# Performance work log

Hardware: AMD Instinct MI355X
Metric: run time of the kernel (lower is better)

The kernel has to match this reference:

```python
import jax, jax.numpy as jnp
import numpy as np

B, N, CPTS = 16, 4096, 64
M, K, RADIUS = 1024, 32, 0.2
MLP = [64, 64, 128]
EPS = 1e-5  # torch BatchNorm2d default


def setup_inputs() -> dict:
    key = jax.random.key(0)
    ks = jax.random.split(key, 2 + len(MLP))
    inp = {
        "xyz": jax.random.uniform(ks[0], (B, N, 3), dtype=jnp.float32),
        "points": jax.random.normal(ks[1], (B, N, CPTS), dtype=jnp.float32),
    }
    cin = 3 + CPTS
    for i, cout in enumerate(MLP):
        inp[f"W{i}"] = jax.random.normal(ks[2 + i], (cout, cin), dtype=jnp.float32) / np.sqrt(cin)
        inp[f"g{i}"] = jnp.ones((cout,), jnp.float32)
        inp[f"b{i}"] = jnp.zeros((cout,), jnp.float32)
        cin = cout
    return inp


def fps(xyz, m):
    # Farthest point sampling, deterministic start at index 0. Returns (B, m) int32.
    b, n, _ = xyz.shape

    def step(carry, _):
        min_d, far = carry
        cent = jnp.take_along_axis(xyz, far[:, None, None], axis=1)  # (B,1,3)
        d = jnp.sum((xyz - cent) ** 2, axis=-1)                      # (B,N)
        min_d = jnp.minimum(min_d, d)
        return (min_d, jnp.argmax(min_d, axis=-1).astype(jnp.int32)), far

    init = (jnp.full((b, n), 1e10, xyz.dtype), jnp.zeros((b,), jnp.int32))
    _, inds = jax.lax.scan(step, init, None, length=m)
    return inds.T  # (B, m)


def ball_query(xyz, new_xyz, radius, k):
    # Euclidean distances (B,M,N); indices within radius, first-k, pad with first valid.
    d2 = (jnp.sum(new_xyz ** 2, -1)[:, :, None] + jnp.sum(xyz ** 2, -1)[:, None, :]
          - 2.0 * jnp.einsum('bmc,bnc->bmn', new_xyz, xyz))
    dists = jnp.sqrt(jnp.maximum(d2, 0.0))
    n = xyz.shape[1]
    idx = jnp.where(dists > radius, n, jnp.arange(n, dtype=jnp.int32)[None, None, :])
    idx = jnp.sort(idx, axis=-1)[:, :, :k]          # first k in-radius indices (N-padded)
    first = idx[:, :, :1]                           # centroid itself (dist 0) always valid
    return jnp.where(idx == n, first, idx)          # (B, M, k)


def reference(xyz, points, W0, g0, b0, W1, g1, b1, W2, g2, b2):
    bidx = jnp.arange(B)[:, None]
    fps_inds = fps(xyz, M)                          # (B, M)
    new_xyz = xyz[bidx, fps_inds]                   # (B, M, 3)
    g_inds = ball_query(xyz, new_xyz, RADIUS, K)    # (B, M, K)
    bidx2 = jnp.arange(B)[:, None, None]
    grouped_xyz = xyz[bidx2, g_inds] - new_xyz[:, :, None, :]   # (B,M,K,3) local coords
    grouped_pts = points[bidx2, g_inds]                          # (B,M,K,C)
    feats = jnp.concatenate([grouped_xyz, grouped_pts], axis=-1)  # (B,M,K,3+C)

    # 1x1 Conv2d (no bias) + BatchNorm2d (training-mode batch stats) + ReLU
    for Wi, gi, bi in ((W0, g0, b0), (W1, g1, b1), (W2, g2, b2)):
        h = jnp.einsum('bmkc,oc->bmko', feats, Wi)
        mean = h.mean(axis=(0, 1, 2))
        var = h.var(axis=(0, 1, 2))
        feats = jax.nn.relu(gi * (h - mean) * jax.lax.rsqrt(var + EPS) + bi)

    new_points = feats.max(axis=2)                  # max-pool over K -> (B, M, 128)
    return new_xyz, new_points, g_inds
```

## Files before the change

kernel.cpp:

```cpp
#include <hip/hip_runtime.h>
#include <hip/hip_bf16.h>
#include <cstdint>

#define B_ 16
#define N_ 4096
#define CPTS_ 64
#define M_ 1024
#define K_ 32
#define MF_TOT 2097152

using ushort8 = __attribute__((ext_vector_type(8))) unsigned short;
using bf16x8  = __attribute__((ext_vector_type(8))) short;
using f32x4v  = __attribute__((ext_vector_type(4))) float;

static __device__ __forceinline__ unsigned f2bf(float x){
  unsigned u = __float_as_uint(x);
  return (u + 0x7fffu + ((u >> 16) & 1u)) >> 16;
}
static __device__ __forceinline__ float bf2f(unsigned short u){
  return __uint_as_float(((unsigned)u) << 16);
}

#define DPPMAX(v, ctrl)                                                        \
  do {                                                                         \
    int _t = __builtin_amdgcn_update_dpp(0, __float_as_int(v), (ctrl), 0xf,    \
                                         0xf, true);                           \
    (v) = fmaxf((v), __int_as_float(_t));                                      \
  } while (0)

#define STEP(MD, PX, PY, PZ, C, J)                                             \
  { float dx = PX.C - cx, dy = PY.C - cy, dz = PZ.C - cz;                      \
    float d = dx * dx; d = d + dy * dy; d = d + dz * dz;                       \
    float nm = fminf(MD.C, d); MD.C = nm;                                      \
    if (nm > bv){ bv = nm; bj = (J); } }
#define STEP4(MD, PX, PY, PZ, J0)                                              \
  STEP(MD, PX, PY, PZ, x, J0)                                                  \
  STEP(MD, PX, PY, PZ, y, (J0) + 1)                                            \
  STEP(MD, PX, PY, PZ, z, (J0) + 2)                                            \
  STEP(MD, PX, PY, PZ, w, (J0) + 3)

__global__ __launch_bounds__(256, 1) void fps_kernel(const float* __restrict__ xyz,
                                                     float* __restrict__ newxyz){
#pragma clang fp contract(off)
  __shared__ float xs[N_], ys[N_], zs[N_];
  __shared__ int inds_s[M_];
  __shared__ unsigned long long sv_[2][4];
  const int b = blockIdx.x, tid = threadIdx.x;
  const int lane = tid & 63, wv = tid >> 6;
  const float* xb = xyz + (size_t)b * N_ * 3;
  for (int i = tid; i < N_ * 3; i += 256){
    float v = xb[i];
    int n = i / 3, c = i - n * 3;
    if (c == 0) xs[n] = v; else if (c == 1) ys[n] = v; else zs[n] = v;
  }
  __syncthreads();
  const float4 px0 = *reinterpret_cast<const float4*>(&xs[tid * 16 + 0]);
  const float4 px1 = *reinterpret_cast<const float4*>(&xs[tid * 16 + 4]);
  const float4 px2 = *reinterpret_cast<const float4*>(&xs[tid * 16 + 8]);
  const float4 px3 = *reinterpret_cast<const float4*>(&xs[tid * 16 + 12]);
  const float4 py0 = *reinterpret_cast<const float4*>(&ys[tid * 16 + 0]);
  const float4 py1 = *reinterpret_cast<const float4*>(&ys[tid * 16 + 4]);
  const float4 py2 = *reinterpret_cast<const float4*>(&ys[tid * 16 + 8]);
  const float4 py3 = *reinterpret_cast<const float4*>(&ys[tid * 16 + 12]);
  const float4 pz0 = *reinterpret_cast<const float4*>(&zs[tid * 16 + 0]);
  const float4 pz1 = *reinterpret_cast<const float4*>(&zs[tid * 16 + 4]);
  const float4 pz2 = *reinterpret_cast<const float4*>(&zs[tid * 16 + 8]);
  const float4 pz3 = *reinterpret_cast<const float4*>(&zs[tid * 16 + 12]);
  float4 md0 = make_float4(1e10f, 1e10f, 1e10f, 1e10f);
  float4 md1 = md0, md2 = md0, md3 = md0;
  int far = 0;
  float cx = xs[0], cy = ys[0], cz = zs[0];
  for (int m = 0; m < M_; ++m){
    if (tid == 0) inds_s[m] = far;
    float bv = -1.0f; int bj = 0;
    STEP4(md0, px0, py0, pz0, 0)
    STEP4(md1, px1, py1, pz1, 4)
    STEP4(md2, px2, py2, pz2, 8)
    STEP4(md3, px3, py3, pz3, 12)
    float wm = bv;
    DPPMAX(wm, 0x111);
    DPPMAX(wm, 0x112);
    DPPMAX(wm, 0x114);
    DPPMAX(wm, 0x118);
    DPPMAX(wm, 0x142);
    DPPMAX(wm, 0x143);
    const float wmax = __int_as_float(
        __builtin_amdgcn_readlane(__float_as_int(wm), 63));
    unsigned long long tied = __ballot(bv == wmax);
    const int winlane = (int)__builtin_ctzll(tied);
    const int sl = m & 1;
    if (lane == winlane){
      int wn = tid * 16 + bj;
      sv_[sl][wv] = ((unsigned long long)__float_as_uint(wmax) << 32)
                  | (unsigned)(4095 - wn);
    }
    __syncthreads();
    unsigned long long p0 = sv_[sl][0], p1 = sv_[sl][1], p2 = sv_[sl][2], p3 = sv_[sl][3];
    if (p1 > p0) p0 = p1;
    if (p3 > p2) p2 = p3;
    if (p2 > p0) p0 = p2;
    far = 4095 - (int)(p0 & 0xffffffffu);
    cx = xs[far]; cy = ys[far]; cz = zs[far];
  }
  __syncthreads();
  for (int t = tid; t < M_; t += 256){
    int id = inds_s[t];
    size_t o = ((size_t)b * M_ + t) * 3;
    newxyz[o] = xs[id]; newxyz[o + 1] = ys[id]; newxyz[o + 2] = zs[id];
  }
}

__global__ __launch_bounds__(256) void phi_kernel(const float* __restrict__ xyz,
                                                  const float* __restrict__ points,
                                                  const float* __restrict__ W,
                                                  float* __restrict__ phi){
  __shared__ __align__(16) float Wt[67][64];
  __shared__ __align__(16) float ft[67][128];
  const int tid = threadIdx.x, blk = blockIdx.x;
  const int p0 = blk * 128;
  for (int i = tid; i < 67 * 64; i += 256){
    int o = i / 67, c = i - o * 67;
    Wt[c][o] = W[i];
  }
  const int sl = tid >> 1, half = tid & 1;
  const int p = p0 + sl;
  const float* ps = points + (size_t)p * CPTS_ + half * 32;
  #pragma unroll
  for (int j = 0; j < 8; ++j){
    float4 v = *reinterpret_cast<const float4*>(ps + j * 4);
    int c = 3 + half * 32 + j * 4;
    ft[c][sl] = v.x; ft[c + 1][sl] = v.y; ft[c + 2][sl] = v.z; ft[c + 3][sl] = v.w;
  }
  if (half == 0){
    const float* xp = xyz + (size_t)p * 3;
    ft[0][sl] = xp[0]; ft[1][sl] = xp[1]; ft[2][sl] = xp[2];
  }
  __syncthreads();
  const int sg = tid & 31, og = tid >> 5;
  float acc[4][8];
  #pragma unroll
  for (int i = 0; i < 4; ++i)
    #pragma unroll
    for (int o = 0; o < 8; ++o) acc[i][o] = 0.0f;
  #pragma unroll 2
  for (int c = 0; c < 67; ++c){
    float4 f = *reinterpret_cast<const float4*>(&ft[c][sg * 4]);
    float4 w0 = *reinterpret_cast<const float4*>(&Wt[c][og * 8]);
    float4 w1 = *reinterpret_cast<const float4*>(&Wt[c][og * 8 + 4]);
    const float fv[4] = {f.x, f.y, f.z, f.w};
    #pragma unroll
    for (int i = 0; i < 4; ++i){
      acc[i][0] += fv[i] * w0.x; acc[i][1] += fv[i] * w0.y;
      acc[i][2] += fv[i] * w0.z; acc[i][3] += fv[i] * w0.w;
      acc[i][4] += fv[i] * w1.x; acc[i][5] += fv[i] * w1.y;
      acc[i][6] += fv[i] * w1.z; acc[i][7] += fv[i] * w1.w;
    }
  }
  #pragma unroll
  for (int i = 0; i < 4; ++i){
    float* dst = phi + (size_t)(p0 + sg * 4 + i) * 64 + og * 8;
    *reinterpret_cast<float4*>(dst)     = make_float4(acc[i][0], acc[i][1], acc[i][2], acc[i][3]);
    *reinterpret_cast<float4*>(dst + 4) = make_float4(acc[i][4], acc[i][5], acc[i][6], acc[i][7]);
  }
}

__global__ __launch_bounds__(256) void ballq_psi_kernel(const float* __restrict__ xyz,
                                                        const float* __restrict__ newxyz,
                                                        int* __restrict__ gi,
                                                        float* __restrict__ gif,
                                                        const float* __restrict__ W0,
                                                        float* __restrict__ psi){
  if (blockIdx.x >= 4096){
    const int mi = (blockIdx.x - 4096) * 256 + threadIdx.x;
    const float x = newxyz[(size_t)mi * 3];
    const float y = newxyz[(size_t)mi * 3 + 1];
    const float z = newxyz[(size_t)mi * 3 + 2];
    float* dst = psi + (size_t)mi * 64;
    #pragma unroll
    for (int o4 = 0; o4 < 16; ++o4){
      float v[4];
      #pragma unroll
      for (int e = 0; e < 4; ++e){
        int o = o4 * 4 + e;
        v[e] = fmaf(z, W0[o * 67 + 2], fmaf(y, W0[o * 67 + 1], x * W0[o * 67]));
      }
      *reinterpret_cast<float4*>(dst + o4 * 4) = make_float4(v[0], v[1], v[2], v[3]);
    }
    return;
  }
  const int gw = (blockIdx.x * 256 + threadIdx.x) >> 6;
  const int lane = threadIdx.x & 63;
  const int b = gw >> 10, m = gw & 1023;
  const float* xb = xyz + (size_t)b * N_ * 3;
  const size_t no = (size_t)b * M_ + m;
  const float cx = newxyz[no * 3], cy = newxyz[no * 3 + 1], cz = newxyz[no * 3 + 2];
  const float sm = fmaf(cz, cz, fmaf(cy, cy, cx * cx));
  int total = 0, first_idx = 0; bool havef = false;
  int*   gd = gi  + no * K_;
  float* fd = gif + no * K_;
  for (int ch = 0; ch < 64 && total < K_; ++ch){
    const int n = ch * 64 + lane;
    const float x = xb[n * 3], y = xb[n * 3 + 1], z = xb[n * 3 + 2];
    const float sn = fmaf(z, z, fmaf(y, y, x * x));
    const float dt = fmaf(z, cz, fmaf(y, cy, x * cx));
    float d2 = (sm + sn) - 2.0f * dt;
    float dist = sqrtf(fmaxf(d2, 0.0f));
    bool pred = !(dist > 0.2f);
    unsigned long long mask = __ballot(pred);
    if (!havef && mask){ havef = true; first_idx = ch * 64 + (int)__builtin_ctzll(mask); }
    if (pred){
      int rank = total + (int)__popcll(mask & ((1ull << lane) - 1ull));
      if (rank < K_){ gd[rank] = n; fd[rank] = (float)n; }
    }
    total += (int)__popcll(mask);
  }
  if (total < K_ && lane >= total && lane < K_){ gd[lane] = first_idx; fd[lane] = (float)first_idx; }
}

__global__ __launch_bounds__(256) void stats0_kernel(const float* __restrict__ phi,
                                                     const float* __restrict__ psi,
                                                     const int* __restrict__ gi,
                                                     float* __restrict__ part){
  __shared__ int gidx[128];
  __shared__ float psm[4][64];
  const int tid = threadIdx.x, blk = blockIdx.x;
  const size_t s0 = (size_t)blk * 128;
  const int b  = (int)(s0 >> 15);
  const int m0 = ((int)(s0 & 32767)) >> 5;
  if (tid < 128) gidx[tid] = gi[(size_t)b * 32768 + (size_t)m0 * K_ + tid];
  psm[tid >> 6][tid & 63] =
      psi[((size_t)b * M_ + m0 + (tid >> 6)) * 64 + (tid & 63)];
  __syncthreads();
  const int sg = tid & 31, og = tid >> 5;
  const int mi = sg >> 3;
  float sv[8], sq[8];
  #pragma unroll
  for (int o = 0; o < 8; ++o){ sv[o] = 0.f; sq[o] = 0.f; }
  #pragma unroll
  for (int i = 0; i < 4; ++i){
    const int g = gidx[sg * 4 + i];
    const float* gp = phi + ((size_t)b * N_ + g) * 64 + og * 8;
    float4 a0 = *reinterpret_cast<const float4*>(gp);
    float4 a1 = *reinterpret_cast<const float4*>(gp + 4);
    const float pv[8] = {a0.x, a0.y, a0.z, a0.w, a1.x, a1.y, a1.z, a1.w};
    #pragma unroll
    for (int o = 0; o < 8; ++o){
      float v = pv[o] - psm[mi][og * 8 + o];
      sv[o] += v; sq[o] += v * v;
    }
  }
  #pragma unroll
  for (int off = 1; off < 32; off <<= 1){
    #pragma unroll
    for (int o = 0; o < 8; ++o){
      sv[o] += __shfl_xor(sv[o], off);
      sq[o] += __shfl_xor(sq[o], off);
    }
  }
  if (sg == 0){
    #pragma unroll
    for (int o = 0; o < 8; ++o){
      int ch = og * 8 + o;
      part[(size_t)(ch * 2) * 4096 + blk]     = sv[o];
      part[(size_t)(ch * 2 + 1) * 4096 + blk] = sq[o];
    }
  }
}

__global__ __launch_bounds__(256) void mlp1_mfma(
    const float* __restrict__ phi, const float* __restrict__ psi,
    const int* __restrict__ gi, const float* __restrict__ bn0,
    const float* __restrict__ W1,
    unsigned short* __restrict__ h1, float* __restrict__ part)
{
  __shared__ unsigned short wsh[64 * 72], wsl[64 * 72];
  __shared__ unsigned short fsh[128 * 72], fsl[128 * 72];
  __shared__ int gidx[128];
  __shared__ float psm[4][64];
  const int tid = threadIdx.x, blk = blockIdx.x;
  const size_t s0 = (size_t)blk * 128;
  const int b  = (int)(s0 >> 15);
  const int m0 = ((int)(s0 & 32767)) >> 5;

  for (int i = tid; i < 64 * 64; i += 256){
    int o = i >> 6, c = i & 63;
    float f = W1[i];
    unsigned hb = f2bf(f);
    float res = f - bf2f((unsigned short)hb);
    wsh[o * 72 + c] = (unsigned short)hb;
    wsl[o * 72 + c] = (unsigned short)f2bf(res);
  }
  if (tid < 128) gidx[tid] = gi[(size_t)b * 32768 + (size_t)m0 * K_ + tid];
  psm[tid >> 6][tid & 63] =
      psi[((size_t)b * M_ + m0 + (tid >> 6)) * 64 + (tid & 63)];
  __syncthreads();
  {
    const int sl = tid >> 1, half = tid & 1;
    const int g = gidx[sl];
    const int mi = sl >> 5;
    const float* gp = phi + ((size_t)b * N_ + g) * 64 + half * 32;
    #pragma unroll
    for (int jj = 0; jj < 4; ++jj){
      float4 v0 = *reinterpret_cast<const float4*>(gp + jj * 8);
      float4 v1 = *reinterpret_cast<const float4*>(gp + jj * 8 + 4);
      const float vv[8] = {v0.x, v0.y, v0.z, v0.w, v1.x, v1.y, v1.z, v1.w};
      ushort8 ph, pl;
      #pragma unroll
      for (int e = 0; e < 8; ++e){
        int c = half * 32 + jj * 8 + e;
        float f = fmaxf((vv[e] - psm[mi][c]) * bn0[c] + bn0[64 + c], 0.0f);
        unsigned hb = f2bf(f);
        float res = f - bf2f((unsigned short)hb);
        ph[e] = (unsigned short)hb;
        pl[e] = (unsigned short)f2bf(res);
      }
      *reinterpret_cast<ushort8*>(&fsh[sl * 72 + half * 32 + jj * 8]) = ph;
      *reinterpret_cast<ushort8*>(&fsl[sl * 72 + half * 32 + jj * 8]) = pl;
    }
  }
  __syncthreads();

  const int l = tid & 63, w = tid >> 6;
  const int col = l & 15, g4 = l >> 4;
  const int ch = w * 16 + col;

  bf16x8 bh[2], bl[2];
  #pragma unroll
  for (int ks = 0; ks < 2; ++ks){
    int a = ch * 72 + ks * 32 + g4 * 8;
    bh[ks] = *reinterpret_cast<const bf16x8*>(&wsh[a]);
    bl[ks] = *reinterpret_cast<const bf16x8*>(&wsl[a]);
  }

  f32x4v acc[8];
  #pragma unroll
  for (int st = 0; st < 8; ++st) acc[st] = (f32x4v){0.f, 0.f, 0.f, 0.f};

  #pragma unroll
  for (int st = 0; st < 8; ++st){
    #pragma unroll
    for (int ks = 0; ks < 2; ++ks){
      int a = (st * 16 + col) * 72 + ks * 32 + g4 * 8;
      bf16x8 ah = *reinterpret_cast<const bf16x8*>(&fsh[a]);
      bf16x8 al = *reinterpret_cast<const bf16x8*>(&fsl[a]);
      acc[st] = __builtin_amdgcn_mfma_f32_16x16x32_bf16(ah, bh[ks], acc[st], 0, 0, 0);
      acc[st] = __builtin_amdgcn_mfma_f32_16x16x32_bf16(ah, bl[ks], acc[st], 0, 0, 0);
      acc[st] = __builtin_amdgcn_mfma_f32_16x16x32_bf16(al, bh[ks], acc[st], 0, 0, 0);
    }
  }

  #pragma unroll
  for (int st = 0; st < 8; ++st){
    size_t sbase = s0 + st * 16 + g4 * 4;
    #pragma unroll
    for (int r = 0; r < 4; ++r)
      h1[(sbase + r) * 64 + ch] = (unsigned short)f2bf(acc[st][r]);
  }

  float sv = 0.f, sq = 0.f;
  #pragma unroll
  for (int st = 0; st < 8; ++st){
    f32x4v a = acc[st];
    float t0 = a[0], t1 = a[1], t2 = a[2], t3 = a[3];
    sv += ((t0 + t1) + t2) + t3;
    sq += ((t0 * t0 + t1 * t1) + t2 * t2) + t3 * t3;
  }
  sv += __shfl_xor(sv, 16); sv += __shfl_xor(sv, 32);
  sq += __shfl_xor(sq, 16); sq += __shfl_xor(sq, 32);
  if (g4 == 0){
    part[(size_t)(ch * 2) * 4096 + blk]     = sv;
    part[(size_t)(ch * 2 + 1) * 4096 + blk] = sq;
  }
}

__global__ __launch_bounds__(256) void mlp2_mfma(
    const unsigned short* __restrict__ h1, const float* __restrict__ bn1,
    const float* __restrict__ W2, float* __restrict__ part,
    float* __restrict__ mxmn)
{
  __shared__ unsigned short wsh[128 * 72], wsl[128 * 72];
  __shared__ unsigned short fsh[128 * 72], fsl[128 * 72];
  const int tid = threadIdx.x, blk = blockIdx.x;
  const size_t s0 = (size_t)blk * 128;

  for (int i = tid; i < 128 * 64; i += 256){
    int o = i >> 6, c = i & 63;
    float f = W2[i];
    unsigned hb = f2bf(f);
    float res = f - bf2f((unsigned short)hb);
    wsh[o * 72 + c] = (unsigned short)hb;
    wsl[o * 72 + c] = (unsigned short)f2bf(res);
  }
  {
    const int sl = tid >> 1, c0 = (tid & 1) * 32;
    const unsigned short* hp = h1 + (s0 + sl) * 64 + c0;
    #pragma unroll
    for (int j = 0; j < 4; ++j){
      ushort8 raw = *reinterpret_cast<const ushort8*>(hp + j * 8);
      ushort8 ph, pl;
      #pragma unroll
      for (int e = 0; e < 8; ++e){
        int c = c0 + j * 8 + e;
        float f = fmaxf(bf2f(raw[e]) * bn1[c] + bn1[64 + c], 0.0f);
        unsigned hb = f2bf(f);
        float res = f - bf2f((unsigned short)hb);
        ph[e] = (unsigned short)hb;
        pl[e] = (unsigned short)f2bf(res);
      }
      *reinterpret_cast<ushort8*>(&fsh[sl * 72 + c0 + j * 8]) = ph;
      *reinterpret_cast<ushort8*>(&fsl[sl * 72 + c0 + j * 8]) = pl;
    }
  }
  __syncthreads();

  const int l = tid & 63, w = tid >> 6;
  const int col = l & 15, g = l >> 4;

  bf16x8 bh[2][2], bl[2][2];
  #pragma unroll
  for (int ot = 0; ot < 2; ++ot)
    #pragma unroll
    for (int ks = 0; ks < 2; ++ks){
      int a = (w * 32 + ot * 16 + col) * 72 + ks * 32 + g * 8;
      bh[ot][ks] = *reinterpret_cast<const bf16x8*>(&wsh[a]);
      bl[ot][ks] = *reinterpret_cast<const bf16x8*>(&wsl[a]);
    }

  f32x4v acc[8][2];
  #pragma unroll
  for (int st = 0; st < 8; ++st)
    #pragma unroll
    for (int ot = 0; ot < 2; ++ot)
      acc[st][ot] = (f32x4v){0.f, 0.f, 0.f, 0.f};

  #pragma unroll
  for (int st = 0; st < 8; ++st){
    bf16x8 ah[2], al[2];
    #pragma unroll
    for (int ks = 0; ks < 2; ++ks){
      int a = (st * 16 + col) * 72 + ks * 32 + g * 8;
      ah[ks] = *reinterpret_cast<const bf16x8*>(&fsh[a]);
      al[ks] = *reinterpret_cast<const bf16x8*>(&fsl[a]);
    }
    #pragma unroll
    for (int ot = 0; ot < 2; ++ot){
      #pragma unroll
      for (int ks = 0; ks < 2; ++ks){
        acc[st][ot] = __builtin_amdgcn_mfma_f32_16x16x32_bf16(ah[ks], bh[ot][ks], acc[st][ot], 0, 0, 0);
        acc[st][ot] = __builtin_amdgcn_mfma_f32_16x16x32_bf16(ah[ks], bl[ot][ks], acc[st][ot], 0, 0, 0);
        acc[st][ot] = __builtin_amdgcn_mfma_f32_16x16x32_bf16(al[ks], bh[ot][ks], acc[st][ot], 0, 0, 0);
      }
    }
  }

  #pragma unroll
  for (int ot = 0; ot < 2; ++ot){
    const int ch = w * 32 + ot * 16 + col;
    float sv = 0.f, sq = 0.f;
    float mxm[4], mnm[4];
    #pragma unroll
    for (int j = 0; j < 4; ++j){ mxm[j] = -1e30f; mnm[j] = 1e30f; }
    #pragma unroll
    for (int st = 0; st < 8; ++st){
      f32x4v a = acc[st][ot];
      float t0 = a[0], t1 = a[1], t2 = a[2], t3 = a[3];
      sv += ((t0 + t1) + t2) + t3;
      sq += ((t0 * t0 + t1 * t1) + t2 * t2) + t3 * t3;
      float tmx = fmaxf(fmaxf(t0, t1), fmaxf(t2, t3));
      float tmn = fminf(fminf(t0, t1), fminf(t2, t3));
      mxm[st >> 1] = fmaxf(mxm[st >> 1], tmx);
      mnm[st >> 1] = fminf(mnm[st >> 1], tmn);
    }
    sv += __shfl_xor(sv, 16); sv += __shfl_xor(sv, 32);
    sq += __shfl_xor(sq, 16); sq += __shfl_xor(sq, 32);
    #pragma unroll
    for (int j = 0; j < 4; ++j){
      mxm[j] = fmaxf(mxm[j], __shfl_xor(mxm[j], 16));
      mxm[j] = fmaxf(mxm[j], __shfl_xor(mxm[j], 32));
      mnm[j] = fminf(mnm[j], __shfl_xor(mnm[j], 16));
      mnm[j] = fminf(mnm[j], __shfl_xor(mnm[j], 32));
    }
    if (g == 0){
      part[(size_t)(ch * 2) * 4096 + blk]     = sv;
      part[(size_t)(ch * 2 + 1) * 4096 + blk] = sq;
      #pragma unroll
      for (int j = 0; j < 4; ++j){
        size_t mf = (s0 >> 5) + j;
        mxmn[mf * 128 + ch]          = mxm[j];
        mxmn[MF_TOT + mf * 128 + ch] = mnm[j];
      }
    }
  }
}

__global__ __launch_bounds__(256) void reduce_stats(const float* __restrict__ part,
                                                    const float* __restrict__ g,
                                                    const float* __restrict__ bb,
                                                    float* __restrict__ bn, int cout){
  const int ch = blockIdx.x, tid = threadIdx.x;
  float s = 0.f, q = 0.f;
  const float* ps = part + (size_t)(ch * 2) * 4096;
  const float* pq = part + (size_t)(ch * 2 + 1) * 4096;
  for (int i = tid; i < 4096; i += 256){ s += ps[i]; q += pq[i]; }
  #pragma unroll
  for (int off = 1; off < 64; off <<= 1){ s += __shfl_xor(s, off); q += __shfl_xor(q, off); }
  __shared__ float as_[4], aq_[4];
  if ((tid & 63) == 0){ as_[tid >> 6] = s; aq_[tid >> 6] = q; }
  __syncthreads();
  if (tid == 0){
    float S = as_[0] + as_[1] + as_[2] + as_[3];
    float Q = aq_[0] + aq_[1] + aq_[2] + aq_[3];
    const float cnt = 524288.0f;
    float mean = S / cnt;
    float var  = Q / cnt - mean * mean;
    float sc = g[ch] / sqrtf(var + 1e-5f);
    bn[ch] = sc;
    bn[cout + ch] = bb[ch] - mean * sc;
  }
}

__global__ __launch_bounds__(256) void bn_minmax_finish(const float* __restrict__ mxmn,
                                                        const float* __restrict__ bn2,
                                                        float* __restrict__ out){
  const int i = blockIdx.x * 256 + threadIdx.x;
  const int ch = i & 127;
  const float a = bn2[ch], sh = bn2[128 + ch];
  const float mx = mxmn[i], mn = mxmn[MF_TOT + i];
  out[i] = fmaxf(fmaxf(mx * a + sh, mn * a + sh), 0.0f);
}

extern "C" void kernel_launch(void* const* d_in, const int* in_sizes, int n_in,
                              void* d_out, int out_size, void* d_ws, size_t ws_size,
                              hipStream_t stream){
  (void)in_sizes; (void)n_in; (void)out_size; (void)ws_size;
  const float* xyz    = (const float*)d_in[0];
  const float* points = (const float*)d_in[1];
  const float* W0 = (const float*)d_in[2];
  const float* g0 = (const float*)d_in[3];
  const float* b0 = (const float*)d_in[4];
  const float* W1 = (const float*)d_in[5];
  const float* g1 = (const float*)d_in[6];
  const float* b1 = (const float*)d_in[7];
  const float* W2 = (const float*)d_in[8];
  const float* g2 = (const float*)d_in[9];
  const float* b2 = (const float*)d_in[10];

  float* out = (float*)d_out;
  float* o_newxyz = out;
  float* o_newpts = out + (size_t)B_ * M_ * 3;
  float* o_gind   = out + (size_t)B_ * M_ * 3 + (size_t)B_ * M_ * 128;

  char* ws = (char*)d_ws;
  int*   gi   = (int*)(ws + 0);
  float* part = (float*)(ws + (2ull << 20));
  float* bn0  = (float*)(ws + (6ull << 20));
  float* bn1  = (float*)(ws + (6ull << 20) + 1024);
  float* bn2  = (float*)(ws + (6ull << 20) + 2048);
  float* phi  = (float*)(ws + (8ull << 20));
  float* psi  = (float*)(ws + (24ull << 20));
  unsigned short* h1 = (unsigned short*)(ws + (28ull << 20));
  float* mxmn = (float*)(ws + (92ull << 20));

  phi_kernel<<<512, 256, 0, stream>>>(xyz, points, W0, phi);
  fps_kernel<<<16, 256, 0, stream>>>(xyz, o_newxyz);
  ballq_psi_kernel<<<4160, 256, 0, stream>>>(xyz, o_newxyz, gi, o_gind, W0, psi);

  stats0_kernel<<<4096, 256, 0, stream>>>(phi, psi, gi, part);
  reduce_stats<<<64, 256, 0, stream>>>(part, g0, b0, bn0, 64);

  mlp1_mfma<<<4096, 256, 0, stream>>>(phi, psi, gi, bn0, W1, h1, part);
  reduce_stats<<<64, 256, 0, stream>>>(part, g1, b1, bn1, 64);

  mlp2_mfma<<<4096, 256, 0, stream>>>(h1, bn1, W2, part, mxmn);
  reduce_stats<<<128, 256, 0, stream>>>(part, g2, b2, bn2, 128);
  bn_minmax_finish<<<MF_TOT / 256, 256, 0, stream>>>(mxmn, bn2, o_newpts);
}
```

Baseline: 876.2 us.

## Fuse phi into FPS launch and fold layer-0 stats into ball query

The phi projection blocks now run in the same launch as the 16 FPS blocks, so phi can fill the idle CUs while the long serial FPS loop runs instead of executing as a separate kernel. The ball query kernel keeps each wave's neighbour indices in shared memory and computes the per-centroid layer-0 sum and sum-of-squares right away, which removes the separate stats0 kernel and its reread of gi. A new row-major reduce kernel reduces these per-wave partials. The cost is a larger partial buffer (16384x64 values each for sum and sum-of-squares) and a gathered phi read per wave inside the ball query kernel.

```diff
diff --git a/kernel.cpp b/kernel.cpp
--- a/kernel.cpp
+++ b/kernel.cpp
@@ -8,6 +8,7 @@
 #define M_ 1024
 #define K_ 32
 #define MF_TOT 2097152
+#define NW_ 16384
 
 using ushort8 = __attribute__((ext_vector_type(8))) unsigned short;
 using bf16x8  = __attribute__((ext_vector_type(8))) short;
@@ -39,137 +40,142 @@
   STEP(MD, PX, PY, PZ, z, (J0) + 2)                                            \
   STEP(MD, PX, PY, PZ, w, (J0) + 3)
 
-__global__ __launch_bounds__(256, 1) void fps_kernel(const float* __restrict__ xyz,
-                                                     float* __restrict__ newxyz){
+__global__ __launch_bounds__(256, 1) void fps_phi_kernel(
+    const float* __restrict__ xyz, float* __restrict__ newxyz,
+    const float* __restrict__ points, const float* __restrict__ W,
+    float* __restrict__ phi){
+  __shared__ __align__(16) char smem[53760];
+  if (blockIdx.x >= 16){
+    float* Wt = (float*)smem;
+    float* ft = (float*)(smem + 17152);
+    const int tid = threadIdx.x, blk = blockIdx.x - 16;
+    const int p0 = blk * 128;
+    for (int i = tid; i < 67 * 64; i += 256){
+      int o = i / 67, c = i - o * 67;
+      Wt[c * 64 + o] = W[i];
+    }
+    const int sl = tid >> 1, half = tid & 1;
+    const int p = p0 + sl;
+    const float* ps = points + (size_t)p * CPTS_ + half * 32;
+    #pragma unroll
+    for (int j = 0; j < 8; ++j){
+      float4 v = *reinterpret_cast<const float4*>(ps + j * 4);
+      int c = 3 + half * 32 + j * 4;
+      ft[c * 128 + sl] = v.x; ft[(c + 1) * 128 + sl] = v.y;
+      ft[(c + 2) * 128 + sl] = v.z; ft[(c + 3) * 128 + sl] = v.w;
+    }
+    if (half == 0){
+      const float* xp = xyz + (size_t)p * 3;
+      ft[0 * 128 + sl] = xp[0]; ft[1 * 128 + sl] = xp[1]; ft[2 * 128 + sl] = xp[2];
+    }
+    __syncthreads();
+    const int sg = tid & 31, og = tid >> 5;
+    float acc[4][8];
+    #pragma unroll
+    for (int i = 0; i < 4; ++i)
+      #pragma unroll
+      for (int o = 0; o < 8; ++o) acc[i][o] = 0.0f;
+    #pragma unroll 2
+    for (int c = 0; c < 67; ++c){
+      float4 f = *reinterpret_cast<const float4*>(&ft[c * 128 + sg * 4]);
+      float4 w0 = *reinterpret_cast<const float4*>(&Wt[c * 64 + og * 8]);
+      float4 w1 = *reinterpret_cast<const float4*>(&Wt[c * 64 + og * 8 + 4]);
+      const float fv[4] = {f.x, f.y, f.z, f.w};
+      #pragma unroll
+      for (int i = 0; i < 4; ++i){
+        acc[i][0] += fv[i] * w0.x; acc[i][1] += fv[i] * w0.y;
+        acc[i][2] += fv[i] * w0.z; acc[i][3] += fv[i] * w0.w;
+        acc[i][4] += fv[i] * w1.x; acc[i][5] += fv[i] * w1.y;
+        acc[i][6] += fv[i] * w1.z; acc[i][7] += fv[i] * w1.w;
+      }
+    }
+    #pragma unroll
+    for (int i = 0; i < 4; ++i){
+      float* dst = phi + (size_t)(p0 + sg * 4 + i) * 64 + og * 8;
+      *reinterpret_cast<float4*>(dst)     = make_float4(acc[i][0], acc[i][1], acc[i][2], acc[i][3]);
+      *reinterpret_cast<float4*>(dst + 4) = make_float4(acc[i][4], acc[i][5], acc[i][6], acc[i][7]);
+    }
+    return;
+  }
+  {
 #pragma clang fp contract(off)
-  __shared__ float xs[N_], ys[N_], zs[N_];
-  __shared__ int inds_s[M_];
-  __shared__ unsigned long long sv_[2][4];
-  const int b = blockIdx.x, tid = threadIdx.x;
-  const int lane = tid & 63, wv = tid >> 6;
-  const float* xb = xyz + (size_t)b * N_ * 3;
-  for (int i = tid; i < N_ * 3; i += 256){
-    float v = xb[i];
-    int n = i / 3, c = i - n * 3;
-    if (c == 0) xs[n] = v; else if (c == 1) ys[n] = v; else zs[n] = v;
-  }
-  __syncthreads();
-  const float4 px0 = *reinterpret_cast<const float4*>(&xs[tid * 16 + 0]);
-  const float4 px1 = *reinterpret_cast<const float4*>(&xs[tid * 16 + 4]);
-  const float4 px2 = *reinterpret_cast<const float4*>(&xs[tid * 16 + 8]);
-  const float4 px3 = *reinterpret_cast<const float4*>(&xs[tid * 16 + 12]);
-  const float4 py0 = *reinterpret_cast<const float4*>(&ys[tid * 16 + 0]);
-  const float4 py1 = *reinterpret_cast<const float4*>(&ys[tid * 16 + 4]);
-  const float4 py2 = *reinterpret_cast<const float4*>(&ys[tid * 16 + 8]);
-  const float4 py3 = *reinterpret_cast<const float4*>(&ys[tid * 16 + 12]);
-  const float4 pz0 = *reinterpret_cast<const float4*>(&zs[tid * 16 + 0]);
-  const float4 pz1 = *reinterpret_cast<const float4*>(&zs[tid * 16 + 4]);
-  const float4 pz2 = *reinterpret_cast<const float4*>(&zs[tid * 16 + 8]);
-  const float4 pz3 = *reinterpret_cast<const float4*>(&zs[tid * 16 + 12]);
-  float4 md0 = make_float4(1e10f, 1e10f, 1e10f, 1e10f);
-  float4 md1 = md0, md2 = md0, md3 = md0;
-  int far = 0;
-  float cx = xs[0], cy = ys[0], cz = zs[0];
-  for (int m = 0; m < M_; ++m){
-    if (tid == 0) inds_s[m] = far;
-    float bv = -1.0f; int bj = 0;
-    STEP4(md0, px0, py0, pz0, 0)
-    STEP4(md1, px1, py1, pz1, 4)
-    STEP4(md2, px2, py2, pz2, 8)
-    STEP4(md3, px3, py3, pz3, 12)
-    float wm = bv;
-    DPPMAX(wm, 0x111);
-    DPPMAX(wm, 0x112);
-    DPPMAX(wm, 0x114);
-    DPPMAX(wm, 0x118);
-    DPPMAX(wm, 0x142);
-    DPPMAX(wm, 0x143);
-    const float wmax = __int_as_float(
-        __builtin_amdgcn_readlane(__float_as_int(wm), 63));
-    unsigned long long tied = __ballot(bv == wmax);
-    const int winlane = (int)__builtin_ctzll(tied);
-    const int sl = m & 1;
-    if (lane == winlane){
-      int wn = tid * 16 + bj;
-      sv_[sl][wv] = ((unsigned long long)__float_as_uint(wmax) << 32)
-                  | (unsigned)(4095 - wn);
+    float* xs = (float*)smem;
+    float* ys = (float*)(smem + 16384);
+    float* zs = (float*)(smem + 32768);
+    int* inds_s = (int*)(smem + 49152);
+    unsigned long long* sv_ = (unsigned long long*)(smem + 53248);
+    const int b = blockIdx.x, tid = threadIdx.x;
+    const int lane = tid & 63, wv = tid >> 6;
+    const float* xb = xyz + (size_t)b * N_ * 3;
+    for (int i = tid; i < N_ * 3; i += 256){
+      float v = xb[i];
+      int n = i / 3, c = i - n * 3;
+      if (c == 0) xs[n] = v; else if (c == 1) ys[n] = v; else zs[n] = v;
     }
     __syncthreads();
-    unsigned long long p0 = sv_[sl][0], p1 = sv_[sl][1], p2 = sv_[sl][2], p3 = sv_[sl][3];
-    if (p1 > p0) p0 = p1;
-    if (p3 > p2) p2 = p3;
-    if (p2 > p0) p0 = p2;
-    far = 4095 - (int)(p0 & 0xffffffffu);
-    cx = xs[far]; cy = ys[far]; cz = zs[far];
-  }
-  __syncthreads();
-  for (int t = tid; t < M_; t += 256){
-    int id = inds_s[t];
-    size_t o = ((size_t)b * M_ + t) * 3;
-    newxyz[o] = xs[id]; newxyz[o + 1] = ys[id]; newxyz[o + 2] = zs[id];
-  }
-}
-
-__global__ __launch_bounds__(256) void phi_kernel(const float* __restrict__ xyz,
-                                                  const float* __restrict__ points,
-                                                  const float* __restrict__ W,
-                                                  float* __restrict__ phi){
-  __shared__ __align__(16) float Wt[67][64];
-  __shared__ __align__(16) float ft[67][128];
-  const int tid = threadIdx.x, blk = blockIdx.x;
-  const int p0 = blk * 128;
-  for (int i = tid; i < 67 * 64; i += 256){
-    int o = i / 67, c = i - o * 67;
-    Wt[c][o] = W[i];
-  }
-  const int sl = tid >> 1, half = tid & 1;
-  const int p = p0 + sl;
-  const float* ps = points + (size_t)p * CPTS_ + half * 32;
-  #pragma unroll
-  for (int j = 0; j < 8; ++j){
-    float4 v = *reinterpret_cast<const float4*>(ps + j * 4);
-    int c = 3 + half * 32 + j * 4;
-    ft[c][sl] = v.x; ft[c + 1][sl] = v.y; ft[c + 2][sl] = v.z; ft[c + 3][sl] = v.w;
-  }
-  if (half == 0){
-    const float* xp = xyz + (size_t)p * 3;
-    ft[0][sl] = xp[0]; ft[1][sl] = xp[1]; ft[2][sl] = xp[2];
-  }
-  __syncthreads();
-  const int sg = tid & 31, og = tid >> 5;
-  float acc[4][8];
-  #pragma unroll
-  for (int i = 0; i < 4; ++i)
-    #pragma unroll
-    for (int o = 0; o < 8; ++o) acc[i][o] = 0.0f;
-  #pragma unroll 2
-  for (int c = 0; c < 67; ++c){
-    float4 f = *reinterpret_cast<const float4*>(&ft[c][sg * 4]);
-    float4 w0 = *reinterpret_cast<const float4*>(&Wt[c][og * 8]);
-    float4 w1 = *reinterpret_cast<const float4*>(&Wt[c][og * 8 + 4]);
-    const float fv[4] = {f.x, f.y, f.z, f.w};
-    #pragma unroll
-    for (int i = 0; i < 4; ++i){
-      acc[i][0] += fv[i] * w0.x; acc[i][1] += fv[i] * w0.y;
-      acc[i][2] += fv[i] * w0.z; acc[i][3] += fv[i] * w0.w;
-      acc[i][4] += fv[i] * w1.x; acc[i][5] += fv[i] * w1.y;
-      acc[i][6] += fv[i] * w1.z; acc[i][7] += fv[i] * w1.w;
-    }
-  }
-  #pragma unroll
-  for (int i = 0; i < 4; ++i){
-    float* dst = phi + (size_t)(p0 + sg * 4 + i) * 64 + og * 8;
-    *reinterpret_cast<float4*>(dst)     = make_float4(acc[i][0], acc[i][1], acc[i][2], acc[i][3]);
-    *reinterpret_cast<float4*>(dst + 4) = make_float4(acc[i][4], acc[i][5], acc[i][6], acc[i][7]);
-  }
-}
-
-__global__ __launch_bounds__(256) void ballq_psi_kernel(const float* __restrict__ xyz,
-                                                        const float* __restrict__ newxyz,
-                                                        int* __restrict__ gi,
-                                                        float* __restrict__ gif,
-                                                        const float* __restrict__ W0,
-                                                        float* __restrict__ psi){
+    const float4 px0 = *reinterpret_cast<const float4*>(&xs[tid * 16 + 0]);
+    const float4 px1 = *reinterpret_cast<const float4*>(&xs[tid * 16 + 4]);
+    const float4 px2 = *reinterpret_cast<const float4*>(&xs[tid * 16 + 8]);
+    const float4 px3 = *reinterpret_cast<const float4*>(&xs[tid * 16 + 12]);
+    const float4 py0 = *reinterpret_cast<const float4*>(&ys[tid * 16 + 0]);
+    const float4 py1 = *reinterpret_cast<const float4*>(&ys[tid * 16 + 4]);
+    const float4 py2 = *reinterpret_cast<const float4*>(&ys[tid * 16 + 8]);
+    const float4 py3 = *reinterpret_cast<const float4*>(&ys[tid * 16 + 12]);
+    const float4 pz0 = *reinterpret_cast<const float4*>(&zs[tid * 16 + 0]);
+    const float4 pz1 = *reinterpret_cast<const float4*>(&zs[tid * 16 + 4]);
+    const float4 pz2 = *reinterpret_cast<const float4*>(&zs[tid * 16 + 8]);
+    const float4 pz3 = *reinterpret_cast<const float4*>(&zs[tid * 16 + 12]);
+    float4 md0 = make_float4(1e10f, 1e10f, 1e10f, 1e10f);
+    float4 md1 = md0, md2 = md0, md3 = md0;
+    int far = 0;
+    float cx = xs[0], cy = ys[0], cz = zs[0];
+    for (int m = 0; m < M_; ++m){
+      if (tid == 0) inds_s[m] = far;
+      float bv = -1.0f; int bj = 0;
+      STEP4(md0, px0, py0, pz0, 0)
+      STEP4(md1, px1, py1, pz1, 4)
+      STEP4(md2, px2, py2, pz2, 8)
+      STEP4(md3, px3, py3, pz3, 12)
+      float wm = bv;
+      DPPMAX(wm, 0x111);
+      DPPMAX(wm, 0x112);
+      DPPMAX(wm, 0x114);
+      DPPMAX(wm, 0x118);
+      DPPMAX(wm, 0x142);
+      DPPMAX(wm, 0x143);
+      const float wmax = __int_as_float(
+          __builtin_amdgcn_readlane(__float_as_int(wm), 63));
+      unsigned long long tied = __ballot(bv == wmax);
+      const int winlane = (int)__builtin_ctzll(tied);
+      const int sl = m & 1;
+      if (lane == winlane){
+        int wn = tid * 16 + bj;
+        sv_[sl * 4 + wv] = ((unsigned long long)__float_as_uint(wmax) << 32)
+                         | (unsigned)(4095 - wn);
+      }
+      __syncthreads();
+      unsigned long long p0 = sv_[sl * 4 + 0], p1 = sv_[sl * 4 + 1];
+      unsigned long long p2 = sv_[sl * 4 + 2], p3 = sv_[sl * 4 + 3];
+      if (p1 > p0) p0 = p1;
+      if (p3 > p2) p2 = p3;
+      if (p2 > p0) p0 = p2;
+      far = 4095 - (int)(p0 & 0xffffffffu);
+      cx = xs[far]; cy = ys[far]; cz = zs[far];
+    }
+    __syncthreads();
+    for (int t = tid; t < M_; t += 256){
+      int id = inds_s[t];
+      size_t o = ((size_t)b * M_ + t) * 3;
+      newxyz[o] = xs[id]; newxyz[o + 1] = ys[id]; newxyz[o + 2] = zs[id];
+    }
+  }
+}
+
+__global__ __launch_bounds__(256) void ballq_stats_kernel(
+    const float* __restrict__ xyz, const float* __restrict__ newxyz,
+    int* __restrict__ gi, float* __restrict__ gif,
+    const float* __restrict__ W0, float* __restrict__ psi,
+    const float* __restrict__ phi, float* __restrict__ part0){
   if (blockIdx.x >= 4096){
     const int mi = (blockIdx.x - 4096) * 256 + threadIdx.x;
     const float x = newxyz[(size_t)mi * 3];
@@ -188,6 +194,8 @@
     }
     return;
   }
+  __shared__ int sidx[4][K_];
+  const int wvb = threadIdx.x >> 6;
   const int gw = (blockIdx.x * 256 + threadIdx.x) >> 6;
   const int lane = threadIdx.x & 63;
   const int b = gw >> 10, m = gw & 1023;
@@ -210,60 +218,51 @@
     if (!havef && mask){ havef = true; first_idx = ch * 64 + (int)__builtin_ctzll(mask); }
     if (pred){
       int rank = total + (int)__popcll(mask & ((1ull << lane) - 1ull));
-      if (rank < K_){ gd[rank] = n; fd[rank] = (float)n; }
+      if (rank < K_){ gd[rank] = n; fd[rank] = (float)n; sidx[wvb][rank] = n; }
     }
     total += (int)__popcll(mask);
   }
-  if (total < K_ && lane >= total && lane < K_){ gd[lane] = first_idx; fd[lane] = (float)first_idx; }
-}
-
-__global__ __launch_bounds__(256) void stats0_kernel(const float* __restrict__ phi,
-                                                     const float* __restrict__ psi,
-                                                     const int* __restrict__ gi,
-                                                     float* __restrict__ part){
-  __shared__ int gidx[128];
-  __shared__ float psm[4][64];
-  const int tid = threadIdx.x, blk = blockIdx.x;
-  const size_t s0 = (size_t)blk * 128;
-  const int b  = (int)(s0 >> 15);
-  const int m0 = ((int)(s0 & 32767)) >> 5;
-  if (tid < 128) gidx[tid] = gi[(size_t)b * 32768 + (size_t)m0 * K_ + tid];
-  psm[tid >> 6][tid & 63] =
-      psi[((size_t)b * M_ + m0 + (tid >> 6)) * 64 + (tid & 63)];
+  if (total < K_ && lane >= total && lane < K_){
+    gd[lane] = first_idx; fd[lane] = (float)first_idx; sidx[wvb][lane] = first_idx;
+  }
   __syncthreads();
-  const int sg = tid & 31, og = tid >> 5;
-  const int mi = sg >> 3;
-  float sv[8], sq[8];
-  #pragma unroll
-  for (int o = 0; o < 8; ++o){ sv[o] = 0.f; sq[o] = 0.f; }
-  #pragma unroll
-  for (int i = 0; i < 4; ++i){
-    const int g = gidx[sg * 4 + i];
-    const float* gp = phi + ((size_t)b * N_ + g) * 64 + og * 8;
-    float4 a0 = *reinterpret_cast<const float4*>(gp);
-    float4 a1 = *reinterpret_cast<const float4*>(gp + 4);
-    const float pv[8] = {a0.x, a0.y, a0.z, a0.w, a1.x, a1.y, a1.z, a1.w};
-    #pragma unroll
-    for (int o = 0; o < 8; ++o){
-      float v = pv[o] - psm[mi][og * 8 + o];
-      sv[o] += v; sq[o] += v * v;
-    }
-  }
-  #pragma unroll
-  for (int off = 1; off < 32; off <<= 1){
-    #pragma unroll
-    for (int o = 0; o < 8; ++o){
-      sv[o] += __shfl_xor(sv[o], off);
-      sq[o] += __shfl_xor(sq[o], off);
-    }
-  }
-  if (sg == 0){
-    #pragma unroll
-    for (int o = 0; o < 8; ++o){
-      int ch = og * 8 + o;
-      part[(size_t)(ch * 2) * 4096 + blk]     = sv[o];
-      part[(size_t)(ch * 2 + 1) * 4096 + blk] = sq[o];
-    }
+  const float wa = W0[lane * 67], wb = W0[lane * 67 + 1], wc = W0[lane * 67 + 2];
+  const float psil = fmaf(cz, wc, fmaf(cy, wb, cx * wa));
+  float sv = 0.f, sq = 0.f;
+  const float* pb = phi + (size_t)b * N_ * 64;
+  #pragma unroll 8
+  for (int k = 0; k < K_; ++k){
+    float v = pb[(size_t)sidx[wvb][k] * 64 + lane] - psil;
+    sv += v; sq += v * v;
+  }
+  part0[(size_t)gw * 64 + lane] = sv;
+  part0[(size_t)NW_ * 64 + (size_t)gw * 64 + lane] = sq;
+}
+
+__global__ __launch_bounds__(256) void reduce_stats_rm(const float* __restrict__ pa,
+                                                       const float* __restrict__ g,
+                                                       const float* __restrict__ bb,
+                                                       float* __restrict__ bn, int cout){
+  const int ch = blockIdx.x, tid = threadIdx.x;
+  float s = 0.f, q = 0.f;
+  for (int i = tid; i < NW_; i += 256){
+    s += pa[(size_t)i * 64 + ch];
+    q += pa[(size_t)NW_ * 64 + (size_t)i * 64 + ch];
+  }
+  #pragma unroll
+  for (int off = 1; off < 64; off <<= 1){ s += __shfl_xor(s, off); q += __shfl_xor(q, off); }
+  __shared__ float as_[4], aq_[4];
+  if ((tid & 63) == 0){ as_[tid >> 6] = s; aq_[tid >> 6] = q; }
+  __syncthreads();
+  if (tid == 0){
+    float S = as_[0] + as_[1] + as_[2] + as_[3];
+    float Q = aq_[0] + aq_[1] + aq_[2] + aq_[3];
+    const float cnt = 524288.0f;
+    float mean = S / cnt;
+    float var  = Q / cnt - mean * mean;
+    float sc = g[ch] / sqrtf(var + 1e-5f);
+    bn[ch] = sc;
+    bn[cout + ch] = bb[ch] - mean * sc;
   }
 }
 
@@ -560,13 +559,12 @@
   float* psi  = (float*)(ws + (24ull << 20));
   unsigned short* h1 = (unsigned short*)(ws + (28ull << 20));
   float* mxmn = (float*)(ws + (92ull << 20));
-
-  phi_kernel<<<512, 256, 0, stream>>>(xyz, points, W0, phi);
-  fps_kernel<<<16, 256, 0, stream>>>(xyz, o_newxyz);
-  ballq_psi_kernel<<<4160, 256, 0, stream>>>(xyz, o_newxyz, gi, o_gind, W0, psi);
-
-  stats0_kernel<<<4096, 256, 0, stream>>>(phi, psi, gi, part);
-  reduce_stats<<<64, 256, 0, stream>>>(part, g0, b0, bn0, 64);
+  float* part0 = (float*)(ws + (108ull << 20));
+
+  fps_phi_kernel<<<528, 256, 0, stream>>>(xyz, o_newxyz, points, W0, phi);
+  ballq_stats_kernel<<<4160, 256, 0, stream>>>(xyz, o_newxyz, gi, o_gind,
+                                               W0, psi, phi, part0);
+  reduce_stats_rm<<<64, 256, 0, stream>>>(part0, g0, b0, bn0, 64);
 
   mlp1_mfma<<<4096, 256, 0, stream>>>(phi, psi, gi, bn0, W1, h1, part);
   reduce_stats<<<64, 256, 0, stream>>>(part, g1, b1, bn1, 64);
```

Measured after the change: 901.6 us. +2.9%, slower.
